# Optimization experiments

Hardware: AMD Instinct MI355X
Metric: run time of the kernel (lower is better)

Reference implementation:

```python
import jax, jax.numpy as jnp
import numpy as np

SEQ, B, OBS, H = 128, 256, 64, 1024

def setup_inputs() -> dict:
    key = jax.random.key(0)
    ks = jax.random.split(key, 16)
    s = 0.03  # keep weights small so tanh/sigmoid stay in a sane range
    n = lambda k, shape, sc=s: jax.random.normal(k, shape, jnp.float32) * sc
    return {
        "x": jax.random.normal(ks[0], (SEQ * B, OBS), jnp.float32),
        "done": jax.random.randint(ks[1], (SEQ * B,), 0, 2).astype(jnp.int32),
        "h0": n(ks[2], (2, B, H), 0.1),
        "c0": n(ks[3], (2, B, H), 0.1),
        "W_ih0": n(ks[4], (4 * H, OBS)),
        "W_hh0": n(ks[5], (4 * H, H)),
        "b_ih0": jnp.zeros((4 * H,), jnp.float32),
        "b_hh0": jnp.zeros((4 * H,), jnp.float32),
        "W_ih1": n(ks[6], (4 * H, H)),
        "W_hh1": n(ks[7], (4 * H, H)),
        "b_ih1": jnp.zeros((4 * H,), jnp.float32),
        "b_hh1": jnp.zeros((4 * H,), jnp.float32),
        "ln_g": jnp.ones((H,), jnp.float32),
        "ln_b": jnp.zeros((H,), jnp.float32),
        "W1": n(ks[8], (512, H)),
        "b1": jnp.zeros((512,), jnp.float32),
        "W2": n(ks[9], (128, 512)),
        "b2": jnp.zeros((128,), jnp.float32),
        "W3": n(ks[10], (64, 128)),
        "b3": jnp.zeros((64,), jnp.float32),
        "Wv": n(ks[11], (1, 64)),
        "bv": jnp.zeros((1,), jnp.float32),
    }

def _lstm_cell(xin, h, c, Wih, Whh, bih, bhh):
    # PyTorch gate order: input, forget, cell(g), output
    g = xin @ Wih.T + bih + h @ Whh.T + bhh
    i, f, gg, o = jnp.split(g, 4, axis=-1)
    c2 = jax.nn.sigmoid(f) * c + jax.nn.sigmoid(i) * jnp.tanh(gg)
    h2 = jax.nn.sigmoid(o) * jnp.tanh(c2)
    return h2, c2

def reference(x, done, h0, c0, W_ih0, W_hh0, b_ih0, b_hh0, W_ih1, W_hh1,
              b_ih1, b_hh1, ln_g, ln_b, W1, b1, W2, b2, W3, b3, Wv, bv):
    batch = h0.shape[1]
    obs = x.shape[-1]
    xs = x.reshape(-1, batch, obs)                      # (S, B, obs)
    ds = done.reshape(-1, batch).astype(x.dtype)        # (S, B)

    def step(carry, td):
        h, c = carry                                    # each (2, B, H)
        xt, dt = td
        m = (1.0 - dt)[:, None]                         # reset mask (B, 1)
        h0_, c0_ = _lstm_cell(xt, h[0] * m, c[0] * m, W_ih0, W_hh0, b_ih0, b_hh0)
        h1_, c1_ = _lstm_cell(h0_, h[1] * m, c[1] * m, W_ih1, W_hh1, b_ih1, b_hh1)
        return (jnp.stack([h0_, h1_]), jnp.stack([c0_, c1_])), h1_

    (hN, cN), hs = jax.lax.scan(step, (h0, c0), (xs, ds))
    hidden = hs.reshape(-1, hs.shape[-1])               # (S*B, H)

    # LayerNorm (eps = 1e-5, torch default)
    mu = hidden.mean(-1, keepdims=True)
    var = jnp.mean(jnp.square(hidden - mu), -1, keepdims=True)
    hn = (hidden - mu) * jax.lax.rsqrt(var + 1e-5) * ln_g + ln_b

    a = jax.nn.elu(hn @ W1.T + b1)
    a = jax.nn.elu(a @ W2.T + b2)
    a = jax.nn.elu(a @ W3.T + b3)
    value = a @ Wv.T + bv                               # (S*B, 1)
    return value, hN, cN
```

## Files before the change

kernel.cpp:

```cpp
#include <hip/hip_runtime.h>
#include <cstdint>
#include <cstddef>

typedef unsigned short u16;
typedef __attribute__((ext_vector_type(8))) short short8;
typedef __attribute__((ext_vector_type(4))) float f32x4;
typedef __attribute__((ext_vector_type(4))) unsigned uint4v;

#define SEQ 128
#define BATCH 256
#define HID 1024
#define LSZ 262144

#define MFMA(a,b,c) __builtin_amdgcn_mfma_f32_16x16x32_bf16((a),(b),(c),0,0,0)

__device__ __forceinline__ u16 f2b(float f) {
  union { float f; unsigned u; } v; v.f = f;
  unsigned r = (v.u + 0x7FFFu + ((v.u >> 16) & 1u)) >> 16;
  return (u16)r;
}
__device__ __forceinline__ float b2f(u16 h) {
  union { unsigned u; float f; } v; v.u = ((unsigned)h) << 16; return v.f;
}
__device__ __forceinline__ float sigm(float x){ return 1.f/(1.f + __expf(-x)); }
__device__ __forceinline__ float tanh_f(float x){
  x = fminf(15.f, fmaxf(-15.f, x));
  float e = __expf(2.f*x); return (e-1.f)/(e+1.f);
}
__device__ __forceinline__ float eluf(float x){ return x > 0.f ? x : expm1f(x); }

__device__ __forceinline__ short8 andm(short8 v, unsigned m) {
  uint4v u = __builtin_bit_cast(uint4v, v);
  u &= m;
  return __builtin_bit_cast(short8, u);
}

__device__ __forceinline__ void store_cg(u16* p, short8 v) {
  asm volatile("global_store_dwordx4 %0, %1, off sc0 sc1" :: "v"(p), "v"(v) : "memory");
}
__device__ __forceinline__ void wait_vm0() {
  asm volatile("s_waitcnt vmcnt(0)" ::: "memory");
}
__device__ __forceinline__ void waitgroup(int* f, int tgt) {
  if (threadIdx.x < 64) {
    int idx = threadIdx.x & 31;
    while (__hip_atomic_load(f + idx, __ATOMIC_RELAXED, __HIP_MEMORY_SCOPE_AGENT) < tgt)
      __builtin_amdgcn_s_sleep(1);
  }
  asm volatile("" ::: "memory");
  __builtin_amdgcn_s_barrier();
  __builtin_amdgcn_sched_barrier(0);
}
__device__ __forceinline__ void waitgroup2(int* fa, int ta, int* fb, int tb) {
  if (threadIdx.x < 64) {
    int idx = threadIdx.x & 31;
    int* p  = (threadIdx.x < 32) ? (fa + idx) : (fb + idx);
    int tgt = (threadIdx.x < 32) ? ta : tb;
    while (__hip_atomic_load(p, __ATOMIC_RELAXED, __HIP_MEMORY_SCOPE_AGENT) < tgt)
      __builtin_amdgcn_s_sleep(1);
  }
  asm volatile("" ::: "memory");
  __builtin_amdgcn_s_barrier();
  __builtin_amdgcn_sched_barrier(0);
}

static const size_t OFF_W0F  = 0;
static const size_t OFF_W1F  = 8912896;
static const size_t OFF_XF   = 25690112;
static const size_t OFF_C0   = 30932992;
static const size_t OFF_C1   = 31981568;
static const size_t OFF_H1U  = 33030144;
static const size_t OFF_BS0  = 100663296;
static const size_t OFF_BS1  = 100679680;
static const size_t OFF_MU   = 100697088;
static const size_t OFF_RSTD = 100828160;
static const size_t OFF_W1LN = 100959232;
static const size_t OFF_S1   = 102007808;
static const size_t OFF_B1P  = 102009856;
static const size_t OFF_W2B  = 102011904;
static const size_t OFF_W3B  = 102142976;
static const size_t OFF_A1   = 102159360;
static const size_t OFF_A2   = 0;
static const size_t OFF_A3   = 8912896;
static const size_t OFF_H0U  = 106353664;

__global__ void prep_wf(const float* __restrict__ wih, const float* __restrict__ whh,
                        u16* __restrict__ out, int nkb, int kx) {
  int b = blockIdx.x; int cg = b >> 3, ct = b & 7;
  int g = ct >> 1;
  int n = nkb << 9;
  for (int e = threadIdx.x; e < n; e += 256) {
    int kb = e >> 9, r = e & 511;
    int q = r >> 7, col16 = (r >> 3) & 15, j = r & 7;
    int hl = (ct & 1) * 16 + col16;
    int gr = g * HID + cg * 32 + hl;
    int k = kb * 32 + q * 8 + j;
    float w = (k < kx) ? wih[(size_t)gr * kx + k] : whh[(size_t)gr * HID + (k - kx)];
    out[((size_t)(cg * nkb + kb) * 8 + ct) * 512 + r] = f2b(w);
  }
}

__global__ void prep_w1ln(const float* __restrict__ w1, const float* __restrict__ lng,
                          const float* __restrict__ lnb, const float* __restrict__ b1,
                          u16* __restrict__ w1ln, float* __restrict__ S1, float* __restrict__ b1p) {
  int j = blockIdx.x;
  float s = 0.f, bb = 0.f;
  for (int k = threadIdx.x; k < HID; k += 256) {
    float w = w1[(size_t)j * HID + k];
    u16 q = f2b(w * lng[k]);
    w1ln[(size_t)j * HID + k] = q;
    s += b2f(q);
    bb += w * lnb[k];
  }
  __shared__ float r1[256], r2[256];
  r1[threadIdx.x] = s; r2[threadIdx.x] = bb;
  __syncthreads();
  for (int o = 128; o > 0; o >>= 1) {
    if (threadIdx.x < (unsigned)o) { r1[threadIdx.x] += r1[threadIdx.x+o]; r2[threadIdx.x] += r2[threadIdx.x+o]; }
    __syncthreads();
  }
  if (threadIdx.x == 0) { S1[j] = r1[0]; b1p[j] = b1[j] + r2[0]; }
}

__global__ void prep_misc(const float* bih0, const float* bhh0, const float* bih1, const float* bhh1,
                          const float* x, const float* h0in, const float* c0in,
                          const float* w2, const float* w3,
                          float* bs0, float* bs1, u16* xf, u16* h0u, u16* h1u,
                          float* c0buf, float* c1buf, u16* w2b, u16* w3b, int* flg) {
  size_t i = (size_t)blockIdx.x * blockDim.x + threadIdx.x;
  if (i < 4096) { bs0[i] = bih0[i] + bhh0[i]; return; }
  i -= 4096;
  if (i < 4096) { bs1[i] = bih1[i] + bhh1[i]; return; }
  i -= 4096;
  if (i < 2097152) {
    int o = (int)i;
    int r = o & 511, tile = o >> 9;
    int q = r >> 7, rl = (r >> 3) & 15, j = r & 7;
    int kb = tile & 1, v = tile >> 1;
    int grt = v & 15, t = v >> 4;
    int row = grt * 16 + rl, k = kb * 32 + q * 8 + j;
    xf[o] = f2b(x[((size_t)t * BATCH + row) * 64 + k]);
    return;
  }
  i -= 2097152;
  if (i < 262144) {
    int o = (int)i;
    int r = o & 511, tile = o >> 9;
    int q = r >> 7, rl = (r >> 3) & 15, j = r & 7;
    int grt = tile >> 5, kb = tile & 31;
    int row = grt * 16 + rl, h = kb * 32 + q * 8 + j;
    h0u[o] = f2b(h0in[(size_t)row * HID + h]);
    return;
  }
  i -= 262144;
  if (i < 262144) {
    int o = (int)i;
    int r = o & 511, tile = o >> 9;
    int q = r >> 7, rl = (r >> 3) & 15, j = r & 7;
    int grt = tile >> 5, kb = tile & 31;
    int row = grt * 16 + rl, h = kb * 32 + q * 8 + j;
    h1u[o] = f2b(h0in[LSZ + (size_t)row * HID + h]);
    return;
  }
  i -= 262144;
  if (i < LSZ) { c0buf[i] = c0in[i]; return; }
  i -= LSZ;
  if (i < LSZ) { c1buf[i] = c0in[LSZ + i]; return; }
  i -= LSZ;
  if (i < 65536) { w2b[i] = f2b(w2[i]); return; }
  i -= 65536;
  if (i < 8192) { w3b[i] = f2b(w3[i]); return; }
  i -= 8192;
  if (i < 512) { flg[i] = 0; return; }
}

__global__ __launch_bounds__(256, 2) void lstm_persist(
    const u16* __restrict__ w0f, const u16* __restrict__ w1f, const u16* __restrict__ xf,
    u16* __restrict__ h0u, u16* __restrict__ h1u,
    float* __restrict__ c0b, float* __restrict__ c1b,
    const float* __restrict__ bs0, const float* __restrict__ bs1,
    const int* __restrict__ done, int* __restrict__ flg,
    float* __restrict__ dout)
{
  const int bid = blockIdx.x;
  const int layer = bid >> 8;
  const int rg = (bid >> 5) & 7;
  const int cg = bid & 31;
  const int tid = threadIdx.x;
  const int lane = tid & 63, wv = tid >> 6;
  const int quad = lane >> 4, c16 = lane & 15;
  const int NKB = layer ? 64 : 34;
  const int NC  = layer ? 32 : 17;
  const u16* Wf = layer ? w1f : w0f;
  const float* bs = layer ? bs1 : bs0;
  float* cb = layer ? c1b : c0b;
  int* fl0 = flg;
  int* fl1 = flg + 256;
  int* myf = (layer ? fl1 : fl0) + rg * 32 + cg;
  int* g0 = fl0 + rg * 32;
  int* g1 = fl1 + rg * 32;

  __shared__ __align__(16) float gl[32 * 132];

  for (int t = 0; t < SEQ; ++t) {
    if (layer == 0) {
      if (t >= 1) waitgroup(g0, t);
    } else {
      if (t >= 1) waitgroup2(g0, t + 1, g1, t);
      else        waitgroup(g0, 1);
    }

    unsigned msk[2];
    #pragma unroll
    for (int a = 0; a < 2; ++a) {
      int row = rg * 32 + a * 16 + (lane & 15);
      msk[a] = done[t * BATCH + row] ? 0u : 0xFFFFFFFFu;
    }

    const u16* a_x  = xf  + (size_t)(t * 16 + rg * 2) * 2 * 512 + lane * 8;
    const u16* a_h0r = h0u + (size_t)t * 262144 + (size_t)(rg * 2) * 32 * 512 + lane * 8;
    const u16* a_h0  = h0u + (size_t)(t + 1) * 262144 + (size_t)(rg * 2) * 32 * 512 + lane * 8;
    const u16* a_h1  = h1u + (size_t)t * 262144 + (size_t)(rg * 2) * 32 * 512 + lane * 8;
    const u16* b_w  = Wf + (size_t)(cg * NKB * 8 + wv * 2) * 512 + lane * 8;

    f32x4 acc[2][2];
    #pragma unroll
    for (int a = 0; a < 2; ++a) { acc[a][0] = (f32x4){0,0,0,0}; acc[a][1] = (f32x4){0,0,0,0}; }

    short8 cA[2][2], cB[2][2], nA[2][2], nB[2][2];

#define LOADC(CIN, AA, BB) { \
    int cc = (CIN); if (cc > NC - 1) cc = NC - 1; \
    _Pragma("unroll") for (int kbl = 0; kbl < 2; ++kbl) { \
      int kb = cc * 2 + kbl; \
      if (layer == 0) { \
        if (kb < 2) { \
          _Pragma("unroll") for (int a = 0; a < 2; ++a) \
            AA[kbl][a] = *(const short8*)(a_x + (size_t)(a * 2 + kb) * 512); \
        } else { \
          _Pragma("unroll") for (int a = 0; a < 2; ++a) \
            AA[kbl][a] = andm(*(const short8*)(a_h0r + (size_t)(a * 32 + (kb - 2)) * 512), msk[a]); \
        } \
      } else { \
        if (kb < 32) { \
          _Pragma("unroll") for (int a = 0; a < 2; ++a) \
            AA[kbl][a] = *(const short8*)(a_h0 + (size_t)(a * 32 + kb) * 512); \
        } else { \
          _Pragma("unroll") for (int a = 0; a < 2; ++a) \
            AA[kbl][a] = andm(*(const short8*)(a_h1 + (size_t)(a * 32 + (kb - 32)) * 512), msk[a]); \
        } \
      } \
      _Pragma("unroll") for (int h = 0; h < 2; ++h) \
        BB[kbl][h] = *(const short8*)(b_w + (size_t)(kb * 8 + h) * 512); \
    } }

#define COMPC(AA, BB) { \
    _Pragma("unroll") for (int kbl = 0; kbl < 2; ++kbl) \
      _Pragma("unroll") for (int a = 0; a < 2; ++a) { \
        acc[a][0] = MFMA(AA[kbl][a], BB[kbl][0], acc[a][0]); \
        acc[a][1] = MFMA(AA[kbl][a], BB[kbl][1], acc[a][1]); \
      } }

    LOADC(0, cA, cB)
    int c = 0;
    for (;;) {
      LOADC(c + 1, nA, nB)
      COMPC(cA, cB)
      if (++c == NC) break;
      LOADC(c + 1, cA, cB)
      COMPC(nA, nB)
      if (++c == NC) break;
    }
#undef LOADC
#undef COMPC

    #pragma unroll
    for (int a = 0; a < 2; ++a)
      #pragma unroll
      for (int h = 0; h < 2; ++h)
        #pragma unroll
        for (int rgi = 0; rgi < 4; ++rgi)
          gl[(a * 16 + quad * 4 + rgi) * 132 + wv * 32 + h * 16 + c16] = acc[a][h][rgi];
    __syncthreads();

    if (tid < 128) {
      int row = tid >> 2;
      int q = tid & 3;
      int h8 = q * 8;
      int rowg = rg * 32 + row;
      int H0 = cg * 32 + h8;
      const float* glp = gl + row * 132;
      float m = done[t * BATCH + rowg] ? 0.f : 1.f;
      float* cp = cb + (size_t)rowg * HID + H0;
      short8 hv;
      float h2a[8], c2a[8];
      #pragma unroll
      for (int j = 0; j < 8; ++j) {
        float ivv = glp[h8 + j]      + bs[H0 + j];
        float fvv = glp[32 + h8 + j] + bs[HID + H0 + j];
        float gvv = glp[64 + h8 + j] + bs[2*HID + H0 + j];
        float ovv = glp[96 + h8 + j] + bs[3*HID + H0 + j];
        float c2 = sigm(fvv) * (cp[j] * m) + sigm(ivv) * tanh_f(gvv);
        float h2 = sigm(ovv) * tanh_f(c2);
        cp[j] = c2;
        h2a[j] = h2; c2a[j] = c2;
        ((u16*)&hv)[j] = f2b(h2);
      }
      size_t off = (size_t)((rg * 2 + (row >> 4)) * 32 + cg) * 512 + (size_t)(q * 16 + (row & 15)) * 8;
      if (layer == 0) store_cg(h0u + (size_t)(t + 1) * 262144 + off, hv);
      else            store_cg(h1u + (size_t)(t + 1) * 262144 + off, hv);
      if (t == SEQ - 1) {
        float* dh = dout + 32768 + (size_t)layer * LSZ + (size_t)rowg * HID + H0;
        float* dc = dout + 32768 + 2 * LSZ + (size_t)layer * LSZ + (size_t)rowg * HID + H0;
        #pragma unroll
        for (int j = 0; j < 8; ++j) { dh[j] = h2a[j]; dc[j] = c2a[j]; }
      }
    }
    wait_vm0();
    __syncthreads();
    if (tid == 0) __hip_atomic_fetch_add(myf, 1, __ATOMIC_RELAXED, __HIP_MEMORY_SCOPE_AGENT);
  }
}

__global__ void ln_stats(const u16* __restrict__ h1u, float* __restrict__ mu, float* __restrict__ rstd) {
  int R = blockIdx.x * 4 + (threadIdx.x >> 6);
  int l = threadIdx.x & 63;
  int t = R >> 8, brow = R & 255, grt = brow >> 4, rl = brow & 15;
  const u16* base = h1u + (size_t)(t + 1) * 262144 + (size_t)(grt * 32 + (l >> 1)) * 512;
  int q2 = (l & 1) * 2;
  short8 v0 = *(const short8*)(base + (q2 * 16 + rl) * 8);
  short8 v1 = *(const short8*)(base + ((q2 + 1) * 16 + rl) * 8);
  float s = 0.f, q = 0.f;
  #pragma unroll
  for (int e = 0; e < 8; ++e) {
    float a = b2f((u16)v0[e]); s += a; q += a*a;
    float b = b2f((u16)v1[e]); s += b; q += b*b;
  }
  for (int o = 32; o > 0; o >>= 1) { s += __shfl_xor(s, o); q += __shfl_xor(q, o); }
  if (l == 0) {
    float mm = s * (1.f/1024.f);
    float var = q * (1.f/1024.f) - mm*mm;
    mu[R] = mm; rstd[R] = rsqrtf(var + 1e-5f);
  }
}

__global__ __launch_bounds__(512, 4) void mlp_gemm(
    const u16* __restrict__ A, int lda, int amode,
    const u16* __restrict__ B, int K, int N,
    u16* __restrict__ out, int ldo, int mode, int swiz,
    const float* __restrict__ mu, const float* __restrict__ rstd,
    const float* __restrict__ S1v, const float* __restrict__ bias)
{
  int nt, mtb;
  if (swiz) { int p = blockIdx.x * gridDim.y + blockIdx.y; nt = p & 3; mtb = p >> 2; }
  else { nt = blockIdx.x; mtb = blockIdx.y; }
  const int tid = threadIdx.x, lane = tid & 63, wv = tid >> 6;
  const int quad = lane >> 4, c16 = lane & 15;
  __shared__ __align__(16) u16 Am[16384], Bm[16384];
  f32x4 acc[8];
  #pragma unroll
  for (int i = 0; i < 8; ++i) acc[i] = (f32x4){0.f,0.f,0.f,0.f};

  int arow[4], akl[4], bcol[4];
  #pragma unroll
  for (int i = 0; i < 4; ++i) {
    int s = tid + i * 512, sub = s >> 6, lp = s & 63;
    int ks = sub >> 3, u = sub & 7;
    arow[i] = mtb * 128 + u * 16 + (lp & 15);
    akl[i]  = ks * 32 + (lp >> 4) * 8;
    bcol[i] = nt * 128 + u * 16 + (lp & 15);
  }
  short8 vA[4], vB[4];
  const short8 z8 = {0,0,0,0,0,0,0,0};
  const int NCH = K >> 7;
  auto load_stage = [&](int ci) {
    int kc = ci << 7;
    #pragma unroll
    for (int i = 0; i < 4; ++i) {
      if (amode) {
        int R = arow[i], k = kc + akl[i];
        const u16* p = A + (size_t)((R >> 8) + 1) * 262144
                         + (size_t)(((R >> 4) & 15) * 32 + (k >> 5)) * 512
                         + (size_t)((((k >> 3) & 3) * 16 + (R & 15)) * 8);
        vA[i] = *(const short8*)p;
      } else {
        vA[i] = *(const short8*)(A + (size_t)arow[i] * lda + kc + akl[i]);
      }
      vB[i] = (bcol[i] < N) ? *(const short8*)(B + (size_t)bcol[i] * K + kc + akl[i]) : z8;
    }
  };
  load_stage(0);
  for (int ci = 0; ci < NCH; ++ci) {
    #pragma unroll
    for (int i = 0; i < 4; ++i) {
      *(short8*)&Am[(size_t)(tid + i*512) * 8] = vA[i];
      *(short8*)&Bm[(size_t)(tid + i*512) * 8] = vB[i];
    }
    __syncthreads();
    if (ci + 1 < NCH) load_stage(ci + 1);
    #pragma unroll
    for (int ks = 0; ks < 4; ++ks) {
      short8 bf = *(const short8*)&Bm[((ks*8 + wv)*64 + lane) * 8];
      #pragma unroll
      for (int rt = 0; rt < 8; ++rt) {
        short8 af = *(const short8*)&Am[((ks*8 + rt)*64 + lane) * 8];
        acc[rt] = MFMA(af, bf, acc[rt]);
      }
    }
    __syncthreads();
  }
  int col = nt * 128 + wv * 16 + c16;
  if (col < N) {
    #pragma unroll
    for (int rt = 0; rt < 8; ++rt) {
      #pragma unroll
      for (int rgi = 0; rgi < 4; ++rgi) {
        int row = mtb * 128 + rt * 16 + quad * 4 + rgi;
        float v = acc[rt][rgi];
        if (mode == 0) v = v * rstd[row] - mu[row] * rstd[row] * S1v[col] + bias[col];
        else           v = v + bias[col];
        v = eluf(v);
        out[(size_t)row * ldo + col] = f2b(v);
      }
    }
  }
}

__global__ void value_head(const u16* __restrict__ a3, const float* __restrict__ wv,
                           const float* __restrict__ bv, float* __restrict__ dout) {
  int row = blockIdx.x * 256 + threadIdx.x;
  const short8* p = (const short8*)(a3 + (size_t)row * 64);
  float s = bv[0];
  #pragma unroll
  for (int j = 0; j < 8; ++j) {
    short8 v = p[j];
    #pragma unroll
    for (int e = 0; e < 8; ++e) s += b2f((u16)v[e]) * wv[j*8+e];
  }
  dout[row] = s;
}

extern "C" void kernel_launch(void* const* d_in, const int* in_sizes, int n_in,
                              void* d_out, int out_size, void* d_ws, size_t ws_size,
                              hipStream_t stream) {
  (void)in_sizes; (void)n_in; (void)out_size; (void)ws_size;
  const float* x    = (const float*)d_in[0];
  const int*   done = (const int*)d_in[1];
  const float* h0in = (const float*)d_in[2];
  const float* c0in = (const float*)d_in[3];
  const float* wih0 = (const float*)d_in[4];
  const float* whh0 = (const float*)d_in[5];
  const float* bih0 = (const float*)d_in[6];
  const float* bhh0 = (const float*)d_in[7];
  const float* wih1 = (const float*)d_in[8];
  const float* whh1 = (const float*)d_in[9];
  const float* bih1 = (const float*)d_in[10];
  const float* bhh1 = (const float*)d_in[11];
  const float* lng  = (const float*)d_in[12];
  const float* lnb  = (const float*)d_in[13];
  const float* w1   = (const float*)d_in[14];
  const float* b1   = (const float*)d_in[15];
  const float* w2   = (const float*)d_in[16];
  const float* b2   = (const float*)d_in[17];
  const float* w3   = (const float*)d_in[18];
  const float* b3   = (const float*)d_in[19];
  const float* wvp  = (const float*)d_in[20];
  const float* bvp  = (const float*)d_in[21];
  float* dout = (float*)d_out;
  char* ws = (char*)d_ws;

  u16*   w0f  = (u16*)(ws + OFF_W0F);
  u16*   w1f  = (u16*)(ws + OFF_W1F);
  u16*   xf   = (u16*)(ws + OFF_XF);
  u16*   h0u  = (u16*)(ws + OFF_H0U);
  u16*   h1u  = (u16*)(ws + OFF_H1U);
  float* c0b  = (float*)(ws + OFF_C0);
  float* c1b  = (float*)(ws + OFF_C1);
  float* bs0  = (float*)(ws + OFF_BS0);
  float* bs1  = (float*)(ws + OFF_BS1);
  int*   flg  = (int*)(ws + OFF_MU);
  float* mu   = (float*)(ws + OFF_MU);
  float* rstd = (float*)(ws + OFF_RSTD);
  u16*   w1ln = (u16*)(ws + OFF_W1LN);
  float* s1   = (float*)(ws + OFF_S1);
  float* b1p  = (float*)(ws + OFF_B1P);
  u16*   w2b  = (u16*)(ws + OFF_W2B);
  u16*   w3b  = (u16*)(ws + OFF_W3B);
  u16*   a1   = (u16*)(ws + OFF_A1);
  u16*   a2   = (u16*)(ws + OFF_A2);
  u16*   a3   = (u16*)(ws + OFF_A3);

  prep_wf<<<256, 256, 0, stream>>>(wih0, whh0, w0f, 34, 64);
  prep_wf<<<256, 256, 0, stream>>>(wih1, whh1, w1f, 64, 1024);
  prep_w1ln<<<512, 256, 0, stream>>>(w1, lng, lnb, b1, w1ln, s1, b1p);
  prep_misc<<<12610, 256, 0, stream>>>(bih0, bhh0, bih1, bhh1, x, h0in, c0in, w2, w3,
                                       bs0, bs1, xf, h0u, h1u, c0b, c1b, w2b, w3b, flg);

  lstm_persist<<<512, 256, 0, stream>>>(w0f, w1f, xf, h0u, h1u, c0b, c1b,
                                        bs0, bs1, done, flg, dout);

  ln_stats<<<8192, 256, 0, stream>>>(h1u, mu, rstd);
  mlp_gemm<<<dim3(8, 128), 512, 0, stream>>>(h1u, 0, 1, w1ln, 1024, 512, a1, 512, 0, 1, mu, rstd, s1, b1p);
  mlp_gemm<<<dim3(1, 256), 512, 0, stream>>>(a1, 512, 0, w2b, 512, 128, a2, 128, 1, 0, mu, rstd, s1, b2);
  mlp_gemm<<<dim3(1, 256), 512, 0, stream>>>(a2, 128, 0, w3b, 128, 64, a3, 64, 1, 0, mu, rstd, s1, b3);
  value_head<<<128, 256, 0, stream>>>(a3, wvp, bvp, dout);
}
```

Measured before the change: 3.410 ms.

## Retile persistent LSTM blocks to 16 rows x 64 hidden with LDS-staged A operands

```diff
diff --git a/kernel.cpp b/kernel.cpp
--- a/kernel.cpp
+++ b/kernel.cpp
@@ -4,6 +4,7 @@
 
 typedef unsigned short u16;
 typedef __attribute__((ext_vector_type(8))) short short8;
+typedef __attribute__((ext_vector_type(4))) short short4v;
 typedef __attribute__((ext_vector_type(4))) float f32x4;
 typedef __attribute__((ext_vector_type(4))) unsigned uint4v;
 
@@ -14,6 +15,10 @@
 
 #define MFMA(a,b,c) __builtin_amdgcn_mfma_f32_16x16x32_bf16((a),(b),(c),0,0,0)
 
+#define GLDS_NC(g, l) __builtin_amdgcn_global_load_lds( \
+  (__attribute__((address_space(1))) void*)(uintptr_t)(const void*)(g), \
+  (__attribute__((address_space(3))) void*)(unsigned)(uintptr_t)(void*)(l), 16, 0, 0)
+
 __device__ __forceinline__ u16 f2b(float f) {
   union { float f; unsigned u; } v; v.f = f;
   unsigned r = (v.u + 0x7FFFu + ((v.u >> 16) & 1u)) >> 16;
@@ -35,15 +40,15 @@
   return __builtin_bit_cast(short8, u);
 }
 
-__device__ __forceinline__ void store_cg(u16* p, short8 v) {
-  asm volatile("global_store_dwordx4 %0, %1, off sc0 sc1" :: "v"(p), "v"(v) : "memory");
+__device__ __forceinline__ void store_cg2(u16* p, short4v v) {
+  asm volatile("global_store_dwordx2 %0, %1, off sc0 sc1" :: "v"(p), "v"(v) : "memory");
 }
 __device__ __forceinline__ void wait_vm0() {
   asm volatile("s_waitcnt vmcnt(0)" ::: "memory");
 }
 __device__ __forceinline__ void waitgroup(int* f, int tgt) {
   if (threadIdx.x < 64) {
-    int idx = threadIdx.x & 31;
+    int idx = threadIdx.x & 15;
     while (__hip_atomic_load(f + idx, __ATOMIC_RELAXED, __HIP_MEMORY_SCOPE_AGENT) < tgt)
       __builtin_amdgcn_s_sleep(1);
   }
@@ -53,7 +58,7 @@
 }
 __device__ __forceinline__ void waitgroup2(int* fa, int ta, int* fb, int tb) {
   if (threadIdx.x < 64) {
-    int idx = threadIdx.x & 31;
+    int idx = threadIdx.x & 15;
     int* p  = (threadIdx.x < 32) ? (fa + idx) : (fb + idx);
     int tgt = (threadIdx.x < 32) ? ta : tb;
     while (__hip_atomic_load(p, __ATOMIC_RELAXED, __HIP_MEMORY_SCOPE_AGENT) < tgt)
@@ -184,23 +189,25 @@
 {
   const int bid = blockIdx.x;
   const int layer = bid >> 8;
-  const int rg = (bid >> 5) & 7;
-  const int cg = bid & 31;
+  const int rg = (bid >> 4) & 15;
+  const int cg = bid & 15;
   const int tid = threadIdx.x;
   const int lane = tid & 63, wv = tid >> 6;
   const int quad = lane >> 4, c16 = lane & 15;
   const int NKB = layer ? 64 : 34;
-  const int NC  = layer ? 32 : 17;
+  const int NC  = layer ? 16 : 9;
   const u16* Wf = layer ? w1f : w0f;
   const float* bs = layer ? bs1 : bs0;
   float* cb = layer ? c1b : c0b;
   int* fl0 = flg;
   int* fl1 = flg + 256;
-  int* myf = (layer ? fl1 : fl0) + rg * 32 + cg;
-  int* g0 = fl0 + rg * 32;
-  int* g1 = fl1 + rg * 32;
-
-  __shared__ __align__(16) float gl[32 * 132];
+  int* myf = (layer ? fl1 : fl0) + rg * 16 + cg;
+  int* g0 = fl0 + rg * 16;
+  int* g1 = fl1 + rg * 16;
+
+  __shared__ __align__(16) float gl[16 * 260];
+  u16* smem = (u16*)gl;
+
 
   for (int t = 0; t < SEQ; ++t) {
     if (layer == 0) {
@@ -210,110 +217,129 @@
       else        waitgroup(g0, 1);
     }
 
-    unsigned msk[2];
-    #pragma unroll
-    for (int a = 0; a < 2; ++a) {
-      int row = rg * 32 + a * 16 + (lane & 15);
-      msk[a] = done[t * BATCH + row] ? 0u : 0xFFFFFFFFu;
-    }
-
-    const u16* a_x  = xf  + (size_t)(t * 16 + rg * 2) * 2 * 512 + lane * 8;
-    const u16* a_h0r = h0u + (size_t)t * 262144 + (size_t)(rg * 2) * 32 * 512 + lane * 8;
-    const u16* a_h0  = h0u + (size_t)(t + 1) * 262144 + (size_t)(rg * 2) * 32 * 512 + lane * 8;
-    const u16* a_h1  = h1u + (size_t)t * 262144 + (size_t)(rg * 2) * 32 * 512 + lane * 8;
-    const u16* b_w  = Wf + (size_t)(cg * NKB * 8 + wv * 2) * 512 + lane * 8;
-
-    f32x4 acc[2][2];
-    #pragma unroll
-    for (int a = 0; a < 2; ++a) { acc[a][0] = (f32x4){0,0,0,0}; acc[a][1] = (f32x4){0,0,0,0}; }
-
-    short8 cA[2][2], cB[2][2], nA[2][2], nB[2][2];
-
-#define LOADC(CIN, AA, BB) { \
-    int cc = (CIN); if (cc > NC - 1) cc = NC - 1; \
-    _Pragma("unroll") for (int kbl = 0; kbl < 2; ++kbl) { \
-      int kb = cc * 2 + kbl; \
-      if (layer == 0) { \
-        if (kb < 2) { \
-          _Pragma("unroll") for (int a = 0; a < 2; ++a) \
-            AA[kbl][a] = *(const short8*)(a_x + (size_t)(a * 2 + kb) * 512); \
-        } else { \
-          _Pragma("unroll") for (int a = 0; a < 2; ++a) \
-            AA[kbl][a] = andm(*(const short8*)(a_h0r + (size_t)(a * 32 + (kb - 2)) * 512), msk[a]); \
-        } \
-      } else { \
-        if (kb < 32) { \
-          _Pragma("unroll") for (int a = 0; a < 2; ++a) \
-            AA[kbl][a] = *(const short8*)(a_h0 + (size_t)(a * 32 + kb) * 512); \
-        } else { \
-          _Pragma("unroll") for (int a = 0; a < 2; ++a) \
-            AA[kbl][a] = andm(*(const short8*)(a_h1 + (size_t)(a * 32 + (kb - 32)) * 512), msk[a]); \
-        } \
-      } \
-      _Pragma("unroll") for (int h = 0; h < 2; ++h) \
-        BB[kbl][h] = *(const short8*)(b_w + (size_t)(kb * 8 + h) * 512); \
-    } }
-
-#define COMPC(AA, BB) { \
-    _Pragma("unroll") for (int kbl = 0; kbl < 2; ++kbl) \
-      _Pragma("unroll") for (int a = 0; a < 2; ++a) { \
-        acc[a][0] = MFMA(AA[kbl][a], BB[kbl][0], acc[a][0]); \
-        acc[a][1] = MFMA(AA[kbl][a], BB[kbl][1], acc[a][1]); \
-      } }
-
-    LOADC(0, cA, cB)
+    const unsigned mrow = done[t * BATCH + rg * 16 + (lane & 15)] ? 0u : 0xFFFFFFFFu;
+
+    const u16* a_x  = xf  + (size_t)(t * 16 + rg) * 2 * 512 + lane * 8;
+    const u16* a_h0r = h0u + (size_t)t * 262144 + (size_t)rg * 32 * 512 + lane * 8;
+    const u16* a_h0  = h0u + (size_t)(t + 1) * 262144 + (size_t)rg * 32 * 512 + lane * 8;
+    const u16* a_h1  = h1u + (size_t)t * 262144 + (size_t)rg * 32 * 512 + lane * 8;
+
+    auto issueA = [&](int p) {
+      int oc = p; if (oc > NC - 1) oc = NC - 1;
+      int kb = oc * 4 + wv; if (kb > NKB - 1) kb = NKB - 1;
+      u16* lt = &smem[((unsigned)(p & 3)) * 2048 + (unsigned)wv * 512];
+      if (layer == 0) {
+        if (kb < 2) GLDS_NC(a_x + (size_t)kb * 512, lt);
+        else        GLDS_NC(a_h0r + (size_t)(kb - 2) * 512, lt);
+      } else {
+        if (kb < 32) GLDS_NC(a_h0 + (size_t)kb * 512, lt);
+        else         GLDS_NC(a_h1 + (size_t)(kb - 32) * 512, lt);
+      }
+    };
+
+    auto loadB = [&](int p, short8 (&vB)[4][4]) {
+      int oc = p; if (oc > NC - 1) oc = NC - 1;
+      #pragma unroll
+      for (int kbl = 0; kbl < 4; ++kbl) {
+        int kb = oc * 4 + kbl; if (kb > NKB - 1) kb = NKB - 1;
+        #pragma unroll
+        for (int ct = 0; ct < 4; ++ct) {
+          int ctt = wv * 4 + ct;
+          vB[kbl][ct] = *(const short8*)(Wf +
+            ((size_t)((2 * cg + (ctt >> 3)) * NKB + kb) * 8 + (ctt & 7)) * 512 + lane * 8);
+        }
+      }
+    };
+
+    f32x4 acc[4];
+    #pragma unroll
+    for (int ct = 0; ct < 4; ++ct) acc[ct] = (f32x4){0,0,0,0};
+
+    auto comp = [&](int p, short8 (&vB)[4][4]) {
+      int kbc = NKB - p * 4; if (kbc > 4) kbc = 4;
+      const u16* sb = &smem[((unsigned)(p & 3)) * 2048] + lane * 8;
+      #pragma unroll
+      for (int kbl = 0; kbl < 4; ++kbl) if (kbl < kbc) {
+        int kb = p * 4 + kbl;
+        int rec = layer ? (kb >= 32) : (kb >= 2);
+        unsigned mw = rec ? mrow : 0xFFFFFFFFu;
+        short8 af = andm(*(const short8*)(sb + kbl * 512), mw);
+        #pragma unroll
+        for (int ct = 0; ct < 4; ++ct)
+          acc[ct] = MFMA(af, vB[kbl][ct], acc[ct]);
+      }
+    };
+
+    short8 vB0[4][4], vB1[4][4];
+
+    loadB(0, vB0);
+    asm volatile("" ::: "memory");
+    issueA(0);
+    asm volatile("" ::: "memory");
+    issueA(1);
+
+#define CHUNK(CC, VBL, VBU) \
+    loadB((CC) + 1, VBL); \
+    asm volatile("" ::: "memory"); \
+    issueA((CC) + 2); \
+    asm volatile("s_waitcnt vmcnt(17)" ::: "memory"); \
+    __builtin_amdgcn_s_barrier(); \
+    __builtin_amdgcn_sched_barrier(0); \
+    comp((CC), VBU);
+
     int c = 0;
     for (;;) {
-      LOADC(c + 1, nA, nB)
-      COMPC(cA, cB)
-      if (++c == NC) break;
-      LOADC(c + 1, cA, cB)
-      COMPC(nA, nB)
-      if (++c == NC) break;
-    }
-#undef LOADC
-#undef COMPC
-
-    #pragma unroll
-    for (int a = 0; a < 2; ++a)
+      CHUNK(c, vB1, vB0) if (++c == NC) break;
+      CHUNK(c, vB0, vB1) if (++c == NC) break;
+    }
+#undef CHUNK
+
+    wait_vm0();
+    __syncthreads();
+
+    #pragma unroll
+    for (int ct = 0; ct < 4; ++ct) {
+      int ctt = wv * 4 + ct;
+      int g = (ctt & 7) >> 1;
+      int hcol = (ctt >> 3) * 32 + (ctt & 1) * 16 + c16;
       #pragma unroll
-      for (int h = 0; h < 2; ++h)
-        #pragma unroll
-        for (int rgi = 0; rgi < 4; ++rgi)
-          gl[(a * 16 + quad * 4 + rgi) * 132 + wv * 32 + h * 16 + c16] = acc[a][h][rgi];
+      for (int rgi = 0; rgi < 4; ++rgi)
+        gl[(quad * 4 + rgi) * 260 + g * 64 + hcol] = acc[ct][rgi];
+    }
     __syncthreads();
 
-    if (tid < 128) {
-      int row = tid >> 2;
-      int q = tid & 3;
-      int h8 = q * 8;
-      int rowg = rg * 32 + row;
-      int H0 = cg * 32 + h8;
-      const float* glp = gl + row * 132;
+    {
+      int row = tid & 15;
+      int h4 = (tid >> 4) * 4;
+      int rowg = rg * 16 + row;
+      int H0 = cg * 64 + h4;
+      const float* glp = gl + row * 260;
       float m = done[t * BATCH + rowg] ? 0.f : 1.f;
       float* cp = cb + (size_t)rowg * HID + H0;
-      short8 hv;
-      float h2a[8], c2a[8];
+      short4v hv;
+      float h2a[4], c2a[4];
       #pragma unroll
-      for (int j = 0; j < 8; ++j) {
-        float ivv = glp[h8 + j]      + bs[H0 + j];
-        float fvv = glp[32 + h8 + j] + bs[HID + H0 + j];
-        float gvv = glp[64 + h8 + j] + bs[2*HID + H0 + j];
-        float ovv = glp[96 + h8 + j] + bs[3*HID + H0 + j];
+      for (int j = 0; j < 4; ++j) {
+        float ivv = glp[h4 + j]       + bs[H0 + j];
+        float fvv = glp[64 + h4 + j]  + bs[HID + H0 + j];
+        float gvv = glp[128 + h4 + j] + bs[2*HID + H0 + j];
+        float ovv = glp[192 + h4 + j] + bs[3*HID + H0 + j];
         float c2 = sigm(fvv) * (cp[j] * m) + sigm(ivv) * tanh_f(gvv);
         float h2 = sigm(ovv) * tanh_f(c2);
         cp[j] = c2;
         h2a[j] = h2; c2a[j] = c2;
         ((u16*)&hv)[j] = f2b(h2);
       }
-      size_t off = (size_t)((rg * 2 + (row >> 4)) * 32 + cg) * 512 + (size_t)(q * 16 + (row & 15)) * 8;
-      if (layer == 0) store_cg(h0u + (size_t)(t + 1) * 262144 + off, hv);
-      else            store_cg(h1u + (size_t)(t + 1) * 262144 + off, hv);
+      int kbh = H0 >> 5;
+      size_t off = (size_t)(rg * 32 + kbh) * 512 + (size_t)((h4 & 31) >> 3) * 128
+                 + (size_t)row * 8 + (h4 & 7);
+      if (layer == 0) store_cg2(h0u + (size_t)(t + 1) * 262144 + off, hv);
+      else            store_cg2(h1u + (size_t)(t + 1) * 262144 + off, hv);
       if (t == SEQ - 1) {
         float* dh = dout + 32768 + (size_t)layer * LSZ + (size_t)rowg * HID + H0;
         float* dc = dout + 32768 + 2 * LSZ + (size_t)layer * LSZ + (size_t)rowg * HID + H0;
         #pragma unroll
-        for (int j = 0; j < 8; ++j) { dh[j] = h2a[j]; dc[j] = c2a[j]; }
+        for (int j = 0; j < 4; ++j) { dh[j] = h2a[j]; dc[j] = c2a[j]; }
       }
     }
     wait_vm0();
```

Result: no change. 3.437 ms (+0.8%).
